# Optimization experiments

Hardware: AMD Instinct MI355X
Metric: run time of the kernel (lower is better)

The kernel has to match this reference:

```python
import jax, jax.numpy as jnp
import numpy as np

HID = 64  # self.hidden_num

def setup_inputs() -> dict:
    key = jax.random.key(0)
    ks = jax.random.split(key, 6)
    B, C_IN, N, T, C_OUT = 2, 64, 128, 24, 64
    x = jax.random.normal(ks[0], (B, C_IN, N, T), dtype=jnp.float32)
    attention = jax.random.uniform(ks[1], (B, 1, N, N, T), dtype=jnp.float32)
    # agg_fc1: Linear(c_in, 64); agg_fc2: Linear(128, c_out). Store weights as [in, out].
    s1 = 1.0 / np.sqrt(C_IN)
    s2 = 1.0 / np.sqrt(2 * HID)
    W1 = jax.random.uniform(ks[2], (C_IN, HID), jnp.float32, -s1, s1)
    b1 = jax.random.uniform(ks[3], (HID,), jnp.float32, -s1, s1)
    W2 = jax.random.uniform(ks[4], (2 * HID, C_OUT), jnp.float32, -s2, s2)
    b2 = jax.random.uniform(ks[5], (C_OUT,), jnp.float32, -s2, s2)
    return {"x": x, "attention": attention, "W1": W1, "b1": b1, "W2": W2, "b2": b2}

def reference(x, attention, W1, b1, W2, b2):
    # x: [B, H, N, T] -> [B, N, T, H]
    xp = jnp.transpose(x, (0, 2, 3, 1))
    h = xp @ W1 + b1  # [B, N, T, HID]
    # Original: concat(v_feature, h_feature) @ W2 where v=h_i (dim 1=dest i), h=h_j (dim 2=src j).
    # Exact decomposition: message[b,i,j,t] = h[b,i,t]@W2v + h[b,j,t]@W2h + b2,
    # avoiding the O(N^2) concat tensor.
    mv = h @ W2[:HID]   # [B, N, T, C_OUT] (dest part)
    mh = h @ W2[HID:]   # [B, N, T, C_OUT] (src part)
    a = attention[:, 0]  # [B, N(i), N(j), T]
    asum = jnp.sum(a, axis=2)  # [B, N, T]
    upd = asum[..., None] * (mv + b2) + jnp.einsum('bijt,bjtc->bitc', a, mh)
    return jnp.transpose(upd, (0, 3, 1, 2))  # [B, C_OUT, N, T]
```

## Files before the change

kernel.cpp:

```cpp
#include <hip/hip_runtime.h>

constexpr int B_   = 2;
constexpr int CIN  = 64;
constexpr int N    = 128;
constexpr int T    = 24;
constexpr int HID  = 64;
constexpr int COUT = 64;
constexpr int NT   = N * T;
constexpr int BT   = B_ * T;
constexpr int ATT_BLOCKS = B_ * N;
constexpr int XT_BLOCKS  = 32;
constexpr int WF_BLOCKS  = 16;
constexpr int PREP_BLOCKS = ATT_BLOCKS + XT_BLOCKS + WF_BLOCKS;
constexpr int MAIN_BLOCKS = BT * 2;

typedef __attribute__((ext_vector_type(8))) short short8;
typedef __attribute__((ext_vector_type(4))) float f32x4;

__device__ inline unsigned short f2bf(float f) {
    unsigned u = __float_as_uint(f);
    return (unsigned short)((u + 0x7FFFu + ((u >> 16) & 1u)) >> 16);
}

__global__ __launch_bounds__(256) void k_prep(
    const float* __restrict__ x,
    const float* __restrict__ att,
    const float* __restrict__ W1,
    const float* __restrict__ b1,
    const float* __restrict__ W2,
    const float* __restrict__ b2,
    unsigned* __restrict__ xT32,
    unsigned* __restrict__ attT32,
    float* __restrict__ asum_g,
    unsigned short* __restrict__ WfvT,
    unsigned short* __restrict__ WfhT,
    float* __restrict__ bvb2,
    float* __restrict__ bh)
{
    __shared__ __align__(16) unsigned smem_u32[8320];
    const int tid = threadIdx.x;
    const int blk = blockIdx.x;

    if (blk < ATT_BLOCKS) {
        float* ts   = (float*)smem_u32;
        float* psum = ts + 3200;
        const int b = blk >> 7;
        const int i = blk & 127;

        const float* ab = att + ((size_t)b * N + i) * NT;
#pragma unroll
        for (int u = 0; u < 12; ++u) {
            const int idx = tid + 256 * u;
            const int j = idx / T, t = idx - j * T;
            ts[j * 25 + t] = __builtin_nontemporal_load(&ab[idx]);
        }
        __syncthreads();
#pragma unroll
        for (int u = 0; u < 6; ++u) {
            const int e2 = tid + 256 * u;
            const int t = e2 >> 6, jp = e2 & 63, j = jp * 2;
            const unsigned pk = (unsigned)f2bf(ts[j * 25 + t])
                              | ((unsigned)f2bf(ts[(j + 1) * 25 + t]) << 16);
            attT32[((size_t)(b * T + t) * N + i) * 64 + jp] = pk;
        }
        if (tid < 192) {
            const int t = tid >> 3, p = tid & 7;
            float s = 0.f;
#pragma unroll
            for (int q = 0; q < 16; ++q) s += ts[(p * 16 + q) * 25 + t];
            psum[t * 8 + p] = s;
        }
        __syncthreads();
        if (tid < T) {
            float s = 0.f;
#pragma unroll
            for (int p = 0; p < 8; ++p) s += psum[tid * 8 + p];
            asum_g[(size_t)(b * T + tid) * N + i] = s;
        }
    } else if (blk < ATT_BLOCKS + XT_BLOCKS) {
        const int tb = blk - ATT_BLOCKS;
        const int b  = tb >> 4;
        const int n0 = (tb & 15) * 8;
#pragma unroll
        for (int u = 0; u < 12; ++u) {
            const int vidx = tid + 256 * u;
            const int cp = vidx / 48, w48 = vidx - cp * 48;
            const f32x4* vp = (const f32x4*)(x + (size_t)(b * CIN + cp) * NT
                                             + n0 * T + w48 * 4);
            const f32x4 v = __builtin_nontemporal_load(vp);
            smem_u32[cp * 97 + w48 * 2]     = (unsigned)f2bf(v[0]) | ((unsigned)f2bf(v[1]) << 16);
            smem_u32[cp * 97 + w48 * 2 + 1] = (unsigned)f2bf(v[2]) | ((unsigned)f2bf(v[3]) << 16);
        }
        __syncthreads();
#pragma unroll
        for (int v = 0; v < 24; ++v) {
            const int oidx = tid + 256 * v;
            const int t = oidx >> 8, rem = oidx & 255;
            const int n = rem >> 5, cp = rem & 31;
            const int r = n * T + t;
            const unsigned w0 = smem_u32[(2 * cp) * 97 + (r >> 1)];
            const unsigned w1 = smem_u32[(2 * cp + 1) * 97 + (r >> 1)];
            const unsigned v0 = (r & 1) ? (w0 >> 16) : (w0 & 0xFFFFu);
            const unsigned v1 = (r & 1) ? (w1 >> 16) : (w1 & 0xFFFFu);
            xT32[((size_t)(b * T + t) * N + n0 + n) * 32 + cp] = v0 | (v1 << 16);
        }
    } else {
        const int wf   = blk - (ATT_BLOCKS + XT_BLOCKS);
        const int half = wf >> 3;
        const int c0   = (wf & 7) * 8;
        float* sW1 = (float*)smem_u32;
        float* sW2 = sW1 + 64 * 65;
#pragma unroll
        for (int u = 0; u < 16; ++u) {
            const int i = tid + 256 * u;
            const int r = i >> 6, q = i & 63;
            sW1[r * 65 + q] = W1[i];
            sW2[r * 65 + q] = W2[half * 4096 + i];
        }
        __syncthreads();

        const int c = c0 + (tid & 7);
        const int r = tid >> 3;
        float a0 = 0.f, a1 = 0.f;
#pragma unroll
        for (int q = 0; q < 64; ++q) {
            const float w2 = sW2[q * 65 + c];
            a0 += sW1[r * 65 + q] * w2;
            a1 += sW1[(r + 32) * 65 + q] * w2;
        }
        unsigned short* dst = half ? WfhT : WfvT;
        dst[c * 64 + r]      = f2bf(a0);
        dst[c * 64 + r + 32] = f2bf(a1);

        if (tid < 8) {
            const int cb = c0 + tid;
            float s = 0.f;
#pragma unroll
            for (int q = 0; q < 64; ++q) s += b1[q] * sW2[q * 65 + cb];
            if (half) bh[cb] = s;
            else      bvb2[cb] = s + b2[cb];
        }
    }
}

__global__ __launch_bounds__(512) void k_main(
    const unsigned* __restrict__ xT32,
    const unsigned* __restrict__ attT32,
    const unsigned short* __restrict__ WfvT,
    const unsigned short* __restrict__ WfhT,
    const float* __restrict__ bvb2,
    const float* __restrict__ bh,
    const float* __restrict__ asum_g,
    float* __restrict__ out)
{
    __shared__ __align__(16) unsigned x_lds[128][36];
    __shared__ __align__(16) unsigned att_lds[64][68];
    __shared__ __align__(16) unsigned short mh_lds[64][136];

    const int blk   = blockIdx.x;
    const int ihalf = blk & 1;
    const int bt    = blk >> 1;
    const int b     = bt / T;
    const int t     = bt - b * T;

    const int tid  = threadIdx.x;
    const int w    = tid >> 6;
    const int lane = tid & 63;
    const int c16  = lane & 15;
    const int q4   = lane >> 4;

    {
        const uint4* src = (const uint4*)(xT32 + (size_t)bt * 4096);
#pragma unroll
        for (int u = 0; u < 2; ++u) {
            const int vi = tid + 512 * u;
            const uint4 v = src[vi];
            *(uint4*)&x_lds[vi >> 3][(vi & 7) * 4] = v;
        }
    }
    {
        const uint4* src = (const uint4*)(attT32 + ((size_t)bt * 128 + ihalf * 64) * 64);
#pragma unroll
        for (int u = 0; u < 2; ++u) {
            const int vi = tid + 512 * u;
            const uint4 v = src[vi];
            *(uint4*)&att_lds[vi >> 4][(vi & 15) * 4] = v;
        }
    }

    const int ct0 = (w >> 2) * 2;
    short8 wh0[4], wh1[4];
#pragma unroll
    for (int ct = 0; ct < 4; ++ct) {
        wh0[ct] = *(const short8*)(WfhT + (ct * 16 + c16) * 64 + q4 * 8);
        wh1[ct] = *(const short8*)(WfhT + (ct * 16 + c16) * 64 + 32 + q4 * 8);
    }
    short8 wv0[2], wv1[2];
#pragma unroll
    for (int p = 0; p < 2; ++p) {
        wv0[p] = *(const short8*)(WfvT + ((ct0 + p) * 16 + c16) * 64 + q4 * 8);
        wv1[p] = *(const short8*)(WfvT + ((ct0 + p) * 16 + c16) * 64 + 32 + q4 * 8);
    }
    float bhc[4];
#pragma unroll
    for (int ct = 0; ct < 4; ++ct) bhc[ct] = bh[ct * 16 + c16];
    float bvc[2];
#pragma unroll
    for (int p = 0; p < 2; ++p) bvc[p] = bvb2[(ct0 + p) * 16 + c16];

    const int il_base = ihalf * 64 + (w & 3) * 16;
    const f32x4 as4 = *(const f32x4*)(asum_g + (size_t)bt * N + il_base + q4 * 4);

    __syncthreads();

    const short8 a0 = *(const short8*)&x_lds[w * 16 + c16][q4 * 4];
    const short8 a1 = *(const short8*)&x_lds[w * 16 + c16][16 + q4 * 4];
    const int nt_mv = ihalf * 4 + (w & 3);
    const short8 m0 = *(const short8*)&x_lds[nt_mv * 16 + c16][q4 * 4];
    const short8 m1 = *(const short8*)&x_lds[nt_mv * 16 + c16][16 + q4 * 4];

#pragma unroll
    for (int ct = 0; ct < 4; ++ct) {
        f32x4 d = {0.f, 0.f, 0.f, 0.f};
        d = __builtin_amdgcn_mfma_f32_16x16x32_bf16(a0, wh0[ct], d, 0, 0, 0);
        d = __builtin_amdgcn_mfma_f32_16x16x32_bf16(a1, wh1[ct], d, 0, 0, 0);
        uint2 pk;
        pk.x = (unsigned)f2bf(d[0] + bhc[ct]) | ((unsigned)f2bf(d[1] + bhc[ct]) << 16);
        pk.y = (unsigned)f2bf(d[2] + bhc[ct]) | ((unsigned)f2bf(d[3] + bhc[ct]) << 16);
        *(uint2*)&mh_lds[ct * 16 + c16][w * 16 + q4 * 4] = pk;
    }
    f32x4 dv0 = {0.f, 0.f, 0.f, 0.f}, dv1 = {0.f, 0.f, 0.f, 0.f};
    dv0 = __builtin_amdgcn_mfma_f32_16x16x32_bf16(m0, wv0[0], dv0, 0, 0, 0);
    dv0 = __builtin_amdgcn_mfma_f32_16x16x32_bf16(m1, wv1[0], dv0, 0, 0, 0);
    dv1 = __builtin_amdgcn_mfma_f32_16x16x32_bf16(m0, wv0[1], dv1, 0, 0, 0);
    dv1 = __builtin_amdgcn_mfma_f32_16x16x32_bf16(m1, wv1[1], dv1, 0, 0, 0);

    __syncthreads();

    f32x4 acc0 = {0.f, 0.f, 0.f, 0.f}, acc1 = {0.f, 0.f, 0.f, 0.f};
    const int ir = (w & 3) * 16 + c16;
#pragma unroll
    for (int ks = 0; ks < 4; ++ks) {
        const short8 a  = *(const short8*)&att_lds[ir][ks * 16 + q4 * 4];
        const short8 b0 = *(const short8*)&mh_lds[ct0 * 16 + c16][ks * 32 + q4 * 8];
        const short8 b1 = *(const short8*)&mh_lds[(ct0 + 1) * 16 + c16][ks * 32 + q4 * 8];
        acc0 = __builtin_amdgcn_mfma_f32_16x16x32_bf16(a, b0, acc0, 0, 0, 0);
        acc1 = __builtin_amdgcn_mfma_f32_16x16x32_bf16(a, b1, acc1, 0, 0, 0);
    }

    {
        const int cc0 = ct0 * 16 + c16;
        const int cc1 = (ct0 + 1) * 16 + c16;
        float* ob0 = out + (((size_t)b * COUT + cc0) * N + il_base + q4 * 4) * T + t;
        float* ob1 = out + (((size_t)b * COUT + cc1) * N + il_base + q4 * 4) * T + t;
#pragma unroll
        for (int e = 0; e < 4; ++e) {
            ob0[e * T] = acc0[e] + as4[e] * (dv0[e] + bvc[0]);
            ob1[e * T] = acc1[e] + as4[e] * (dv1[e] + bvc[1]);
        }
    }
}

extern "C" void kernel_launch(void* const* d_in, const int* in_sizes, int n_in,
                              void* d_out, int out_size, void* d_ws, size_t ws_size,
                              hipStream_t stream)
{
    const float* x   = (const float*)d_in[0];
    const float* att = (const float*)d_in[1];
    const float* W1  = (const float*)d_in[2];
    const float* b1  = (const float*)d_in[3];
    const float* W2  = (const float*)d_in[4];
    const float* b2  = (const float*)d_in[5];
    float* out = (float*)d_out;

    char* ws = (char*)d_ws;
    unsigned*       xT32   = (unsigned*)ws;
    unsigned*       attT32 = (unsigned*)(ws + 786432);
    float*          asum_g = (float*)(ws + 2359296);
    unsigned short* WfvT   = (unsigned short*)(ws + 2383872);
    unsigned short* WfhT   = (unsigned short*)(ws + 2392064);
    float*          bvb2   = (float*)(ws + 2400256);
    float*          bh     = (float*)(ws + 2400512);

    k_prep<<<PREP_BLOCKS, 256, 0, stream>>>(x, att, W1, b1, W2, b2,
                                            xT32, attT32, asum_g,
                                            WfvT, WfhT, bvb2, bh);
    k_main<<<MAIN_BLOCKS, 512, 0, stream>>>(xT32, attT32,
                                            WfvT, WfhT, bvb2, bh, asum_g, out);
}
```

Before: 18.41 us.

## Fuse attention transpose and row-sum into main kernel, drop attT32 workspace

Removes the attention-processing blocks from the prep kernel. Each main-kernel block now loads its attention slice directly from the fp32 input, converts it to bf16 in LDS, and computes the row sums locally. This avoids writing and rereading a transposed bf16 attention buffer and an asum buffer through global memory. The cost is strided, poorly coalesced global reads of attention (stride T) inside the main kernel, relying on L2 reuse across time-step blocks.

```diff
diff --git a/kernel.cpp b/kernel.cpp
--- a/kernel.cpp
+++ b/kernel.cpp
@@ -8,10 +8,9 @@
 constexpr int COUT = 64;
 constexpr int NT   = N * T;
 constexpr int BT   = B_ * T;
-constexpr int ATT_BLOCKS = B_ * N;
 constexpr int XT_BLOCKS  = 32;
 constexpr int WF_BLOCKS  = 16;
-constexpr int PREP_BLOCKS = ATT_BLOCKS + XT_BLOCKS + WF_BLOCKS;
+constexpr int PREP_BLOCKS = XT_BLOCKS + WF_BLOCKS;
 constexpr int MAIN_BLOCKS = BT * 2;
 
 typedef __attribute__((ext_vector_type(8))) short short8;
@@ -24,14 +23,11 @@
 
 __global__ __launch_bounds__(256) void k_prep(
     const float* __restrict__ x,
-    const float* __restrict__ att,
     const float* __restrict__ W1,
     const float* __restrict__ b1,
     const float* __restrict__ W2,
     const float* __restrict__ b2,
     unsigned* __restrict__ xT32,
-    unsigned* __restrict__ attT32,
-    float* __restrict__ asum_g,
     unsigned short* __restrict__ WfvT,
     unsigned short* __restrict__ WfhT,
     float* __restrict__ bvb2,
@@ -41,46 +37,9 @@
     const int tid = threadIdx.x;
     const int blk = blockIdx.x;
 
-    if (blk < ATT_BLOCKS) {
-        float* ts   = (float*)smem_u32;
-        float* psum = ts + 3200;
-        const int b = blk >> 7;
-        const int i = blk & 127;
-
-        const float* ab = att + ((size_t)b * N + i) * NT;
-#pragma unroll
-        for (int u = 0; u < 12; ++u) {
-            const int idx = tid + 256 * u;
-            const int j = idx / T, t = idx - j * T;
-            ts[j * 25 + t] = __builtin_nontemporal_load(&ab[idx]);
-        }
-        __syncthreads();
-#pragma unroll
-        for (int u = 0; u < 6; ++u) {
-            const int e2 = tid + 256 * u;
-            const int t = e2 >> 6, jp = e2 & 63, j = jp * 2;
-            const unsigned pk = (unsigned)f2bf(ts[j * 25 + t])
-                              | ((unsigned)f2bf(ts[(j + 1) * 25 + t]) << 16);
-            attT32[((size_t)(b * T + t) * N + i) * 64 + jp] = pk;
-        }
-        if (tid < 192) {
-            const int t = tid >> 3, p = tid & 7;
-            float s = 0.f;
-#pragma unroll
-            for (int q = 0; q < 16; ++q) s += ts[(p * 16 + q) * 25 + t];
-            psum[t * 8 + p] = s;
-        }
-        __syncthreads();
-        if (tid < T) {
-            float s = 0.f;
-#pragma unroll
-            for (int p = 0; p < 8; ++p) s += psum[tid * 8 + p];
-            asum_g[(size_t)(b * T + tid) * N + i] = s;
-        }
-    } else if (blk < ATT_BLOCKS + XT_BLOCKS) {
-        const int tb = blk - ATT_BLOCKS;
-        const int b  = tb >> 4;
-        const int n0 = (tb & 15) * 8;
+    if (blk < XT_BLOCKS) {
+        const int b  = blk >> 4;
+        const int n0 = (blk & 15) * 8;
 #pragma unroll
         for (int u = 0; u < 12; ++u) {
             const int vidx = tid + 256 * u;
@@ -105,7 +64,7 @@
             xT32[((size_t)(b * T + t) * N + n0 + n) * 32 + cp] = v0 | (v1 << 16);
         }
     } else {
-        const int wf   = blk - (ATT_BLOCKS + XT_BLOCKS);
+        const int wf   = blk - XT_BLOCKS;
         const int half = wf >> 3;
         const int c0   = (wf & 7) * 8;
         float* sW1 = (float*)smem_u32;
@@ -144,18 +103,19 @@
 }
 
 __global__ __launch_bounds__(512) void k_main(
+    const float* __restrict__ att,
     const unsigned* __restrict__ xT32,
-    const unsigned* __restrict__ attT32,
     const unsigned short* __restrict__ WfvT,
     const unsigned short* __restrict__ WfhT,
     const float* __restrict__ bvb2,
     const float* __restrict__ bh,
-    const float* __restrict__ asum_g,
     float* __restrict__ out)
 {
     __shared__ __align__(16) unsigned x_lds[128][36];
-    __shared__ __align__(16) unsigned att_lds[64][68];
+    __shared__ __align__(16) unsigned short att_lds[64][136];
     __shared__ __align__(16) unsigned short mh_lds[64][136];
+    __shared__ float psum[64][8];
+    __shared__ float asum_f[64];
 
     const int blk   = blockIdx.x;
     const int ihalf = blk & 1;
@@ -179,13 +139,18 @@
         }
     }
     {
-        const uint4* src = (const uint4*)(attT32 + ((size_t)bt * 128 + ihalf * 64) * 64);
-#pragma unroll
-        for (int u = 0; u < 2; ++u) {
-            const int vi = tid + 512 * u;
-            const uint4 v = src[vi];
-            *(uint4*)&att_lds[vi >> 4][(vi & 15) * 4] = v;
-        }
+        const int il = tid >> 3;
+        const int jg = tid & 7;
+        const float* ab = att + ((size_t)b * N + ihalf * 64 + il) * NT + t;
+        float ps = 0.f;
+#pragma unroll
+        for (int jj = 0; jj < 16; ++jj) {
+            const int j = jg * 16 + jj;
+            const float v = ab[(size_t)j * T];
+            ps += v;
+            att_lds[il][j] = f2bf(v);
+        }
+        psum[il][jg] = ps;
     }
 
     const int ct0 = (w >> 2) * 2;
@@ -208,10 +173,14 @@
 #pragma unroll
     for (int p = 0; p < 2; ++p) bvc[p] = bvb2[(ct0 + p) * 16 + c16];
 
-    const int il_base = ihalf * 64 + (w & 3) * 16;
-    const f32x4 as4 = *(const f32x4*)(asum_g + (size_t)bt * N + il_base + q4 * 4);
-
     __syncthreads();
+
+    if (tid < 64) {
+        float s = 0.f;
+#pragma unroll
+        for (int g = 0; g < 8; ++g) s += psum[tid][g];
+        asum_f[tid] = s;
+    }
 
     const short8 a0 = *(const short8*)&x_lds[w * 16 + c16][q4 * 4];
     const short8 a1 = *(const short8*)&x_lds[w * 16 + c16][16 + q4 * 4];
@@ -241,7 +210,7 @@
     const int ir = (w & 3) * 16 + c16;
 #pragma unroll
     for (int ks = 0; ks < 4; ++ks) {
-        const short8 a  = *(const short8*)&att_lds[ir][ks * 16 + q4 * 4];
+        const short8 a  = *(const short8*)&att_lds[ir][ks * 32 + q4 * 8];
         const short8 b0 = *(const short8*)&mh_lds[ct0 * 16 + c16][ks * 32 + q4 * 8];
         const short8 b1 = *(const short8*)&mh_lds[(ct0 + 1) * 16 + c16][ks * 32 + q4 * 8];
         acc0 = __builtin_amdgcn_mfma_f32_16x16x32_bf16(a, b0, acc0, 0, 0, 0);
@@ -249,14 +218,17 @@
     }
 
     {
+        const int il_loc = (w & 3) * 16 + q4 * 4;
+        const int iglob  = ihalf * 64 + il_loc;
         const int cc0 = ct0 * 16 + c16;
         const int cc1 = (ct0 + 1) * 16 + c16;
-        float* ob0 = out + (((size_t)b * COUT + cc0) * N + il_base + q4 * 4) * T + t;
-        float* ob1 = out + (((size_t)b * COUT + cc1) * N + il_base + q4 * 4) * T + t;
+        float* ob0 = out + (((size_t)b * COUT + cc0) * N + iglob) * T + t;
+        float* ob1 = out + (((size_t)b * COUT + cc1) * N + iglob) * T + t;
 #pragma unroll
         for (int e = 0; e < 4; ++e) {
-            ob0[e * T] = acc0[e] + as4[e] * (dv0[e] + bvc[0]);
-            ob1[e * T] = acc1[e] + as4[e] * (dv1[e] + bvc[1]);
+            const float as = asum_f[il_loc + e];
+            ob0[e * T] = acc0[e] + as * (dv0[e] + bvc[0]);
+            ob1[e * T] = acc1[e] + as * (dv1[e] + bvc[1]);
         }
     }
 }
@@ -274,17 +246,14 @@
     float* out = (float*)d_out;
 
     char* ws = (char*)d_ws;
-    unsigned*       xT32   = (unsigned*)ws;
-    unsigned*       attT32 = (unsigned*)(ws + 786432);
-    float*          asum_g = (float*)(ws + 2359296);
-    unsigned short* WfvT   = (unsigned short*)(ws + 2383872);
-    unsigned short* WfhT   = (unsigned short*)(ws + 2392064);
-    float*          bvb2   = (float*)(ws + 2400256);
-    float*          bh     = (float*)(ws + 2400512);
-
-    k_prep<<<PREP_BLOCKS, 256, 0, stream>>>(x, att, W1, b1, W2, b2,
-                                            xT32, attT32, asum_g,
-                                            WfvT, WfhT, bvb2, bh);
-    k_main<<<MAIN_BLOCKS, 512, 0, stream>>>(xT32, attT32,
-                                            WfvT, WfhT, bvb2, bh, asum_g, out);
-}
+    unsigned*       xT32 = (unsigned*)ws;
+    unsigned short* WfvT = (unsigned short*)(ws + 786432);
+    unsigned short* WfhT = (unsigned short*)(ws + 794624);
+    float*          bvb2 = (float*)(ws + 802816);
+    float*          bh   = (float*)(ws + 803072);
+
+    k_prep<<<PREP_BLOCKS, 256, 0, stream>>>(x, W1, b1, W2, b2,
+                                            xT32, WfvT, WfhT, bvb2, bh);
+    k_main<<<MAIN_BLOCKS, 512, 0, stream>>>(att, xT32,
+                                            WfvT, WfhT, bvb2, bh, out);
+}
```

Result: slower. 22.48 us (+22.1%).
